# Optimization experiments

Hardware: AMD Instinct MI355X
Metric: run time of the kernel (lower is better)

The kernel has to match this reference:

```python
import jax, jax.numpy as jnp
import numpy as np

OBS, SEQ = 8, 12          # observed steps, predicted steps (seq_len init arg)
G, P = 96, 16             # scenes x pedestrians per scene (uniform groups)
B = G * P                 # 1536
H, E, BOT, MID = 128, 64, 1024, 512


def setup_inputs() -> dict:
    key = jax.random.key(0)
    ks = jax.random.split(key, 26)
    rn = lambda k, sh, s=0.05: jax.random.normal(k, sh, jnp.float32) * s
    starts = jnp.arange(G, dtype=jnp.int64) * P
    return {
        "obs_traj": rn(ks[0], (OBS, B, 2), 1.0),
        "obs_traj_rel": rn(ks[1], (OBS, B, 2), 1.0),
        "typeID_seq": rn(ks[2], (OBS, B, 1), 1.0),
        "h0": rn(ks[3], (1, B, H), 0.1),
        "c0": rn(ks[4], (1, B, H), 0.1),
        "seq_start_end": jnp.stack([starts, starts + P], axis=1),
        # decoder spatial embedding Linear(2, E)
        "W_emb": rn(ks[5], (E, 2)), "b_emb": rn(ks[6], (E,)),
        # LSTM(E, H) weights, gate order i,f,g,o (PyTorch convention)
        "W_ih": rn(ks[7], (4 * H, E)), "b_ih": rn(ks[8], (4 * H,)),
        "W_hh": rn(ks[9], (4 * H, H)), "b_hh": rn(ks[10], (4 * H,)),
        # hidden2pos Linear(H, 2)
        "W_pos": rn(ks[11], (2, H)), "b_pos": rn(ks[12], (2,)),
        # PoolHiddenNet: spatial_embedding Linear(2, E), mlp_pre_pool [E+H, 512, BOT]
        "Wp_emb": rn(ks[13], (E, 2)), "bp_emb": rn(ks[14], (E,)),
        "Wp1": rn(ks[15], (MID, E + H)), "bp1": rn(ks[16], (MID,)),
        "Wp2": rn(ks[17], (BOT, MID)), "bp2": rn(ks[18], (BOT,)),
        # Decoder mlp [H+BOT, mlp_dim, H]
        "Wm1": rn(ks[19], (1024, H + BOT)), "bm1": rn(ks[20], (1024,)),
        "Wm2": rn(ks[21], (H, 1024)), "bm2": rn(ks[22], (H,)),
    }


def _forward(obs_traj, obs_traj_rel, h0, c0,
             W_emb, b_emb, W_ih, b_ih, W_hh, b_hh, W_pos, b_pos,
             Wp_emb, bp_emb, Wp1, bp1, Wp2, bp2, Wm1, bm1, Wm2, bm2):
    batch = obs_traj.shape[1]

    def pool(h, pos):
        # uniform groups: h_states.view(-1,H)[start:end] == reshape to (G,P,H)
        hh = h.reshape(G, P, H)
        pp = pos.reshape(G, P, 2)
        # torch semantics: row (i,j) holds pos[j]-pos[i] and hidden[j]
        rel = pp[:, None, :, :] - pp[:, :, None, :]          # (G,Pi,Pj,2)
        emb = rel @ Wp_emb.T + bp_emb                        # (G,Pi,Pj,E)
        hb = jnp.broadcast_to(hh[:, None, :, :], (G, P, P, H))
        x = jnp.concatenate([emb, hb], axis=-1)              # (G,Pi,Pj,E+H)
        x = jax.nn.relu(x @ Wp1.T + bp1)
        x = jax.nn.relu(x @ Wp2.T + bp2)                     # (G,Pi,Pj,BOT)
        return x.max(axis=2).reshape(batch, BOT)             # max over neighbors j

    def step(carry, _):
        h, c, last_pos, dec_in = carry
        gates = dec_in @ W_ih.T + b_ih + h @ W_hh.T + b_hh
        i, f, g, o = jnp.split(gates, 4, axis=-1)
        c = jax.nn.sigmoid(f) * c + jax.nn.sigmoid(i) * jnp.tanh(g)
        h = jax.nn.sigmoid(o) * jnp.tanh(c)
        rel_pos = h @ W_pos.T + b_pos                        # (B,2)
        curr_pos = rel_pos + last_pos
        pool_h = pool(h, curr_pos)
        ctx = jnp.concatenate([h, pool_h], axis=-1)          # (B,H+BOT)
        h = jax.nn.relu(jax.nn.relu(ctx @ Wm1.T + bm1) @ Wm2.T + bm2)
        dec_in = rel_pos @ W_emb.T + b_emb
        return (h, c, curr_pos, dec_in), rel_pos

    dec_in0 = obs_traj_rel[-1] @ W_emb.T + b_emb
    carry0 = (h0[0], c0[0], obs_traj[-1], dec_in0)
    (h, c, _, _), rels = jax.lax.scan(step, carry0, None, length=SEQ)
    return rels, h[None]                                     # (SEQ,B,2), (1,B,H)


def reference(obs_traj, obs_traj_rel, typeID_seq, h0, c0, seq_start_end,
              W_emb, b_emb, W_ih, b_ih, W_hh, b_hh, W_pos, b_pos,
              Wp_emb, bp_emb, Wp1, bp1, Wp2, bp2, Wm1, bm1, Wm2, bm2):
    # typeID_seq / seq_start_end unused math-wise (typeID module off; groups uniform)
    return _forward(obs_traj, obs_traj_rel, h0, c0,
                    W_emb, b_emb, W_ih, b_ih, W_hh, b_hh, W_pos, b_pos,
                    Wp_emb, bp_emb, Wp1, bp1, Wp2, bp2, Wm1, bm1, Wm2, bm2)
```

## Files before the change

kernel.cpp:

```cpp
#include <hip/hip_runtime.h>
#include <math.h>

#define OBS 8
#define SEQL 12
#define G 96
#define PP 16
#define B 1536
#define HD 128
#define ED 64
#define BOT 1024
#define MIDD 512
#define CTXD (HD + BOT)
#define MLPH 1024

typedef __attribute__((ext_vector_type(8))) short bf16x8;
typedef __attribute__((ext_vector_type(4))) float f32x4;

__device__ inline short f2bf(float x) {
    union { float f; unsigned u; } v; v.f = x;
    unsigned r = v.u + 0x7fffu + ((v.u >> 16) & 1u);
    return (short)(r >> 16);
}

__global__ void swizzleB_kernel(const float* __restrict__ src, unsigned short* __restrict__ dst,
                                int NT, int K, int total) {
    int u = blockIdx.x * 256 + threadIdx.x;
    if (u >= total) return;
    int l = u & 63; int v = u >> 6; int nt = v % NT; int kt = v / NT;
    int n = nt * 16 + (l & 15);
    int k = kt * 32 + ((l >> 4) << 3);
    const float* s = src + n * K + k;
    float4 s0 = *(const float4*)s;
    float4 s1 = *(const float4*)(s + 4);
    bf16x8 o;
    o[0] = f2bf(s0.x); o[1] = f2bf(s0.y); o[2] = f2bf(s0.z); o[3] = f2bf(s0.w);
    o[4] = f2bf(s1.x); o[5] = f2bf(s1.y); o[6] = f2bf(s1.z); o[7] = f2bf(s1.w);
    *(bf16x8*)(dst + u * 8) = o;
}

__global__ void swizzle_cat_kernel(const float* __restrict__ W_ih, const float* __restrict__ W_hh,
                                   unsigned short* __restrict__ dst) {
    int u = blockIdx.x * 256 + threadIdx.x;
    if (u >= 6 * 32 * 64) return;
    int l = u & 63; int v = u >> 6; int nt = v & 31; int kt = v >> 5;
    int n = nt * 16 + (l & 15);
    int k0 = kt * 32 + ((l >> 4) << 3);
    bf16x8 o;
#pragma unroll
    for (int e = 0; e < 8; ++e) {
        int k = k0 + e;
        float val = (k < ED) ? W_ih[n * ED + k] : W_hh[n * HD + (k - ED)];
        o[e] = f2bf(val);
    }
    *(bf16x8*)(dst + u * 8) = o;
}

__global__ void swizzle_p1_kernel(const float* __restrict__ Wp1, const float* __restrict__ M0,
                                  const float* __restrict__ M1, const float* __restrict__ CV,
                                  unsigned short* __restrict__ dst) {
    int u = blockIdx.x * 256 + threadIdx.x;
    if (u >= 5 * 32 * 64) return;
    int l = u & 63; int v = u >> 6; int nt = v & 31; int kt = v >> 5;
    int n = nt * 16 + (l & 15);
    int k0 = kt * 32 + ((l >> 4) << 3);
    bf16x8 o;
#pragma unroll
    for (int e = 0; e < 8; ++e) {
        int k = k0 + e;
        float val;
        if (k < HD)       val = Wp1[n * (ED + HD) + ED + k];
        else if (k == HD)     val = M0[n];
        else if (k == HD + 1) val = M1[n];
        else if (k == HD + 2) val = CV[n];
        else                  val = 0.f;
        o[e] = f2bf(val);
    }
    *(bf16x8*)(dst + u * 8) = o;
}

__global__ void mcvec_kernel(const float* __restrict__ Wp1, const float* __restrict__ Wp_emb,
                             const float* __restrict__ bp_emb, const float* __restrict__ bp1,
                             float* __restrict__ M0, float* __restrict__ M1, float* __restrict__ CV) {
    int r = blockIdx.x * blockDim.x + threadIdx.x;
    if (r >= MIDD) return;
    float m0 = 0.f, m1 = 0.f, cv = 0.f;
    for (int e = 0; e < ED; ++e) {
        float w = Wp1[r * (ED + HD) + e];
        m0 += w * Wp_emb[e * 2 + 0];
        m1 += w * Wp_emb[e * 2 + 1];
        cv += w * bp_emb[e];
    }
    M0[r] = m0; M1[r] = m1; CV[r] = cv + bp1[r];
}

__global__ void init_kernel(const float* __restrict__ obs_traj, const float* __restrict__ obs_traj_rel,
                            const float* __restrict__ h0, const float* __restrict__ c0,
                            const float* __restrict__ W_emb, const float* __restrict__ b_emb,
                            float* __restrict__ Hb, float* __restrict__ Cb,
                            float* __restrict__ POSb, float* __restrict__ DIN) {
    int b = blockIdx.x;
    int t = threadIdx.x;
    Hb[b * HD + t] = h0[b * HD + t];
    Cb[b * HD + t] = c0[b * HD + t];
    if (t < 2) POSb[b * 2 + t] = obs_traj[((OBS - 1) * B + b) * 2 + t];
    if (t < ED) {
        float rx = obs_traj_rel[((OBS - 1) * B + b) * 2 + 0];
        float ry = obs_traj_rel[((OBS - 1) * B + b) * 2 + 1];
        DIN[b * ED + t] = W_emb[t * 2 + 0] * rx + W_emb[t * 2 + 1] * ry + b_emb[t];
    }
}

__global__ __launch_bounds__(512) void step_kernel(
    const unsigned short* __restrict__ WcatF, const float* __restrict__ b_ih,
    const float* __restrict__ b_hh,
    const float* __restrict__ W_pos, const float* __restrict__ b_pos,
    const float* __restrict__ W_emb, const float* __restrict__ b_emb,
    const unsigned short* __restrict__ Wp1F2,
    float* __restrict__ Hb, float* __restrict__ Cb, float* __restrict__ POSb,
    float* __restrict__ DIN, unsigned short* __restrict__ Hbf,
    float* __restrict__ Ab, float* __restrict__ rel_out) {

    __shared__ unsigned short gf[6 * 64 * 8];
    __shared__ unsigned short a2f[5 * 64 * 8];
    __shared__ float hsh[16 * HD];
    __shared__ float relsh[16][4];

    int gsc = blockIdx.x;
    int t = threadIdx.x;
    int lane = t & 63, w = t >> 6;
    int colid = lane & 15, quad = lane >> 4;

    if (t < 384) {
        int kt = t >> 6;
        int j = lane & 15;
        int b = gsc * PP + j;
        int k0 = kt * 32 + ((lane >> 4) << 3);
        float4 x0, x1;
        if (k0 < ED) {
            const float4* p = (const float4*)(DIN + b * ED + k0);
            x0 = p[0]; x1 = p[1];
        } else {
            const float4* p = (const float4*)(Hb + b * HD + (k0 - ED));
            x0 = p[0]; x1 = p[1];
        }
        bf16x8 o;
        o[0] = f2bf(x0.x); o[1] = f2bf(x0.y); o[2] = f2bf(x0.z); o[3] = f2bf(x0.w);
        o[4] = f2bf(x1.x); o[5] = f2bf(x1.y); o[6] = f2bf(x1.z); o[7] = f2bf(x1.w);
        *(bf16x8*)(gf + t * 8) = o;
    }
    __syncthreads();

    f32x4 acc[4];
#pragma unroll
    for (int gi = 0; gi < 4; ++gi) acc[gi] = (f32x4)0.f;
#pragma unroll
    for (int kt = 0; kt < 6; ++kt) {
        bf16x8 af = *(const bf16x8*)(gf + (kt * 64 + lane) * 8);
#pragma unroll
        for (int gi = 0; gi < 4; ++gi) {
            bf16x8 bfr = *(const bf16x8*)(WcatF + ((kt * 32 + gi * 8 + w) * 64 + lane) * 8);
            acc[gi] = __builtin_amdgcn_mfma_f32_16x16x32_bf16(af, bfr, acc[gi], 0, 0, 0);
        }
    }
    int hcol = w * 16 + colid;
    float bias[4];
#pragma unroll
    for (int gi = 0; gi < 4; ++gi) {
        int n = (gi * 8 + w) * 16 + colid;
        bias[gi] = b_ih[n] + b_hh[n];
    }
#pragma unroll
    for (int r = 0; r < 4; ++r) {
        int row = quad * 4 + r;
        int b = gsc * PP + row;
        float gI = acc[0][r] + bias[0];
        float gF = acc[1][r] + bias[1];
        float gG = acc[2][r] + bias[2];
        float gO = acc[3][r] + bias[3];
        float c = Cb[b * HD + hcol];
        float cn = (1.f / (1.f + expf(-gF))) * c + (1.f / (1.f + expf(-gI))) * tanhf(gG);
        float hn = (1.f / (1.f + expf(-gO))) * tanhf(cn);
        Cb[b * HD + hcol] = cn;
        Hbf[b * HD + hcol] = (unsigned short)f2bf(hn);
        hsh[row * HD + hcol] = hn;
    }
    __syncthreads();

    {
        int row = t >> 5, kk = t & 31;
        float r0 = 0.f, r1 = 0.f;
#pragma unroll
        for (int q = 0; q < 4; ++q) {
            int k = kk + q * 32;
            float hv = hsh[row * HD + k];
            r0 = fmaf(hv, W_pos[k], r0);
            r1 = fmaf(hv, W_pos[HD + k], r1);
        }
#pragma unroll
        for (int m = 16; m >= 1; m >>= 1) {
            r0 += __shfl_xor(r0, m, 64);
            r1 += __shfl_xor(r1, m, 64);
        }
        if (kk == 0) {
            int b = gsc * PP + row;
            r0 += b_pos[0]; r1 += b_pos[1];
            float px = POSb[b * 2 + 0] + r0;
            float py = POSb[b * 2 + 1] + r1;
            POSb[b * 2 + 0] = px; POSb[b * 2 + 1] = py;
            rel_out[b * 2 + 0] = r0; rel_out[b * 2 + 1] = r1;
            relsh[row][0] = r0; relsh[row][1] = r1; relsh[row][2] = px; relsh[row][3] = py;
        }
    }
    __syncthreads();

#pragma unroll
    for (int rep = 0; rep < 2; ++rep) {
        int idx = rep * 512 + t;
        int row = idx >> 6, e = idx & 63;
        int b = gsc * PP + row;
        DIN[b * ED + e] = W_emb[e * 2 + 0] * relsh[row][0] +
                          W_emb[e * 2 + 1] * relsh[row][1] + b_emb[e];
    }
    if (t < 320) {
        int kt = t >> 6;
        int j = lane & 15;
        int k0 = kt * 32 + ((lane >> 4) << 3);
        bf16x8 o;
#pragma unroll
        for (int e = 0; e < 8; ++e) {
            int k = k0 + e;
            float v;
            if (k < HD)            v = hsh[j * HD + k];
            else if (k == HD)      v = relsh[j][2];
            else if (k == HD + 1)  v = relsh[j][3];
            else if (k == HD + 2)  v = 1.f;
            else                   v = 0.f;
            o[e] = f2bf(v);
        }
        *(bf16x8*)(a2f + t * 8) = o;
    }
    __syncthreads();

    f32x4 acc2[4];
#pragma unroll
    for (int q = 0; q < 4; ++q) acc2[q] = (f32x4)0.f;
#pragma unroll
    for (int kt = 0; kt < 5; ++kt) {
        bf16x8 af = *(const bf16x8*)(a2f + (kt * 64 + lane) * 8);
#pragma unroll
        for (int q = 0; q < 4; ++q) {
            bf16x8 bfr = *(const bf16x8*)(Wp1F2 + ((kt * 32 + w * 4 + q) * 64 + lane) * 8);
            acc2[q] = __builtin_amdgcn_mfma_f32_16x16x32_bf16(af, bfr, acc2[q], 0, 0, 0);
        }
    }
#pragma unroll
    for (int q = 0; q < 4; ++q)
#pragma unroll
        for (int r = 0; r < 4; ++r) {
            int b = gsc * PP + quad * 4 + r;
            Ab[b * MIDD + (w * 4 + q) * 16 + colid] = acc2[q][r];
        }
}

__global__ __launch_bounds__(512) void pool_mfma2_kernel(
    const float* __restrict__ Ab, const float* __restrict__ POSb,
    const unsigned short* __restrict__ Wp2F, const float* __restrict__ bp2,
    const float* __restrict__ M0, const float* __restrict__ M1,
    unsigned short* __restrict__ POOLbf) {

    __shared__ float s_lds[4 * MIDD];
    __shared__ unsigned short af_lds[4 * 16 * 64 * 8];

    int bi = blockIdx.x;
    int g = bi >> 2, igrp = bi & 3;
    int t = threadIdx.x, lane = t & 63, w = t >> 6;

#pragma unroll
    for (int rep = 0; rep < 4; ++rep) {
        int idx = rep * 512 + t;
        int ii = idx >> 9, k = idx & 511;
        int i = g * PP + igrp * 4 + ii;
        s_lds[idx] = fmaf(M0[k], POSb[i * 2 + 0], M1[k] * POSb[i * 2 + 1]);
    }
    __syncthreads();
#pragma unroll
    for (int rep = 0; rep < 8; ++rep) {
        int u = rep * 512 + t;
        int ii = u >> 10, kt = (u >> 6) & 15, l = u & 63;
        int j = l & 15, k0 = kt * 32 + ((l >> 4) << 3);
        const float4* ap = (const float4*)(Ab + (g * PP + j) * MIDD + k0);
        float4 a0 = ap[0], a1 = ap[1];
        const float4* sp = (const float4*)(s_lds + ii * MIDD + k0);
        float4 s0 = sp[0], s1 = sp[1];
        bf16x8 o;
        o[0] = f2bf(fmaxf(a0.x - s0.x, 0.f));
        o[1] = f2bf(fmaxf(a0.y - s0.y, 0.f));
        o[2] = f2bf(fmaxf(a0.z - s0.z, 0.f));
        o[3] = f2bf(fmaxf(a0.w - s0.w, 0.f));
        o[4] = f2bf(fmaxf(a1.x - s1.x, 0.f));
        o[5] = f2bf(fmaxf(a1.y - s1.y, 0.f));
        o[6] = f2bf(fmaxf(a1.z - s1.z, 0.f));
        o[7] = f2bf(fmaxf(a1.w - s1.w, 0.f));
        *(bf16x8*)(af_lds + u * 8) = o;
    }
    __syncthreads();

    f32x4 acc[4][8];
#pragma unroll
    for (int ii = 0; ii < 4; ++ii)
#pragma unroll
        for (int n = 0; n < 8; ++n) acc[ii][n] = (f32x4)0.f;

    int ntb = w * 8;
    for (int kt = 0; kt < 16; ++kt) {
        bf16x8 bfr[8];
#pragma unroll
        for (int n = 0; n < 8; ++n)
            bfr[n] = *(const bf16x8*)(Wp2F + ((kt * 64 + ntb + n) * 64 + lane) * 8);
#pragma unroll
        for (int ii = 0; ii < 4; ++ii) {
            bf16x8 af = *(const bf16x8*)(af_lds + ((ii * 16 + kt) * 64 + lane) * 8);
#pragma unroll
            for (int n = 0; n < 8; ++n)
                acc[ii][n] = __builtin_amdgcn_mfma_f32_16x16x32_bf16(af, bfr[n], acc[ii][n], 0, 0, 0);
        }
    }

    int quad = lane >> 4, colid = lane & 15;
#pragma unroll
    for (int ii = 0; ii < 4; ++ii) {
        int i = igrp * 4 + ii;
#pragma unroll
        for (int n = 0; n < 8; ++n) {
            float m = fmaxf(fmaxf(acc[ii][n][0], acc[ii][n][1]),
                            fmaxf(acc[ii][n][2], acc[ii][n][3]));
            m = fmaxf(m, __shfl_xor(m, 16, 64));
            m = fmaxf(m, __shfl_xor(m, 32, 64));
            if (quad == 0) {
                int col = w * 128 + n * 16 + colid;
                float v = fmaxf(m + bp2[col], 0.f);
                POOLbf[(g * PP + i) * BOT + col] = (unsigned short)f2bf(v);
            }
        }
    }
}

__global__ __launch_bounds__(256) void mlp1_mfma_kernel(
    const unsigned short* __restrict__ Hbf, const unsigned short* __restrict__ POOLbf,
    const unsigned short* __restrict__ Wm1F, const float* __restrict__ bm1,
    unsigned short* __restrict__ Y1Mbf) {

    __shared__ unsigned short a_f[16 * 64 * 8];
    int mg = blockIdx.x;
    int ng = blockIdx.y;
    int t = threadIdx.x, lane = t & 63, w = t >> 6;
    int rh = w >> 1, nh = w & 1;

    f32x4 acc[2][2];
#pragma unroll
    for (int a = 0; a < 2; ++a)
#pragma unroll
        for (int b = 0; b < 2; ++b) acc[a][b] = (f32x4)0.f;

    for (int c = 0; c < 9; ++c) {
        __syncthreads();
#pragma unroll
        for (int u0 = 0; u0 < 1024; u0 += 256) {
            int u = u0 + t;
            int rg = u >> 8, kt = (u >> 6) & 3, l = u & 63;
            int row = mg * 64 + rg * 16 + (l & 15);
            int kl = kt * 32 + ((l >> 4) << 3);
            const unsigned short* src = (c == 0) ? (Hbf + row * HD + kl)
                                                 : (POOLbf + row * BOT + (c - 1) * 128 + kl);
            *(bf16x8*)(a_f + u * 8) = *(const bf16x8*)src;
        }
        __syncthreads();
#pragma unroll
        for (int kt = 0; kt < 4; ++kt) {
            int ktg = c * 4 + kt;
            bf16x8 bfr[2];
#pragma unroll
            for (int j = 0; j < 2; ++j) {
                int ntg = ng * 4 + nh * 2 + j;
                bfr[j] = *(const bf16x8*)(Wm1F + ((ktg * 64 + ntg) * 64 + lane) * 8);
            }
#pragma unroll
            for (int ri = 0; ri < 2; ++ri) {
                int rg = rh * 2 + ri;
                bf16x8 af = *(const bf16x8*)(a_f + ((rg * 4 + kt) * 64 + lane) * 8);
#pragma unroll
                for (int j = 0; j < 2; ++j)
                    acc[ri][j] = __builtin_amdgcn_mfma_f32_16x16x32_bf16(af, bfr[j], acc[ri][j], 0, 0, 0);
            }
        }
    }
    int quad = lane >> 4, colid = lane & 15;
#pragma unroll
    for (int ri = 0; ri < 2; ++ri)
#pragma unroll
        for (int j = 0; j < 2; ++j) {
            int col = ng * 64 + (nh * 2 + j) * 16 + colid;
            float bb = bm1[col];
#pragma unroll
            for (int r = 0; r < 4; ++r) {
                int row = mg * 64 + (rh * 2 + ri) * 16 + quad * 4 + r;
                float v = fmaxf(acc[ri][j][r] + bb, 0.f);
                Y1Mbf[row * MLPH + col] = (unsigned short)f2bf(v);
            }
        }
}

__global__ __launch_bounds__(256) void mlp2_mfma_kernel(
    const unsigned short* __restrict__ Y1Mbf, const unsigned short* __restrict__ Wm2F,
    const float* __restrict__ bm2, float* __restrict__ Hb, float* __restrict__ hout) {

    __shared__ unsigned short a_f[32 * 64 * 8];
    int rg = blockIdx.x;
    int t = threadIdx.x, lane = t & 63, w = t >> 6;

#pragma unroll
    for (int u0 = 0; u0 < 2048; u0 += 256) {
        int u = u0 + t;
        int kt = u >> 6, l = u & 63;
        int row = rg * 16 + (l & 15);
        int kl = kt * 32 + ((l >> 4) << 3);
        *(bf16x8*)(a_f + u * 8) = *(const bf16x8*)(Y1Mbf + row * MLPH + kl);
    }
    __syncthreads();

    f32x4 acc[2];
    acc[0] = (f32x4)0.f; acc[1] = (f32x4)0.f;
    for (int kt = 0; kt < 32; ++kt) {
        bf16x8 af = *(const bf16x8*)(a_f + (kt * 64 + lane) * 8);
#pragma unroll
        for (int j = 0; j < 2; ++j) {
            int ntg = w * 2 + j;
            bf16x8 bfr = *(const bf16x8*)(Wm2F + ((kt * 8 + ntg) * 64 + lane) * 8);
            acc[j] = __builtin_amdgcn_mfma_f32_16x16x32_bf16(af, bfr, acc[j], 0, 0, 0);
        }
    }
    int quad = lane >> 4, colid = lane & 15;
#pragma unroll
    for (int j = 0; j < 2; ++j) {
        int col = (w * 2 + j) * 16 + colid;
        float bb = bm2[col];
#pragma unroll
        for (int r = 0; r < 4; ++r) {
            int row = rg * 16 + quad * 4 + r;
            float v = fmaxf(acc[j][r] + bb, 0.f);
            Hb[row * HD + col] = v;
            if (hout) hout[row * HD + col] = v;
        }
    }
}

extern "C" void kernel_launch(void* const* d_in, const int* in_sizes, int n_in,
                              void* d_out, int out_size, void* d_ws, size_t ws_size,
                              hipStream_t stream) {
    const float* obs_traj     = (const float*)d_in[0];
    const float* obs_traj_rel = (const float*)d_in[1];
    const float* h0    = (const float*)d_in[3];
    const float* c0    = (const float*)d_in[4];
    const float* W_emb = (const float*)d_in[6];
    const float* b_emb = (const float*)d_in[7];
    const float* W_ih  = (const float*)d_in[8];
    const float* b_ih  = (const float*)d_in[9];
    const float* W_hh  = (const float*)d_in[10];
    const float* b_hh  = (const float*)d_in[11];
    const float* W_pos = (const float*)d_in[12];
    const float* b_pos = (const float*)d_in[13];
    const float* Wp_emb= (const float*)d_in[14];
    const float* bp_emb= (const float*)d_in[15];
    const float* Wp1   = (const float*)d_in[16];
    const float* bp1   = (const float*)d_in[17];
    const float* Wp2   = (const float*)d_in[18];
    const float* bp2   = (const float*)d_in[19];
    const float* Wm1   = (const float*)d_in[20];
    const float* bm1   = (const float*)d_in[21];
    const float* Wm2   = (const float*)d_in[22];
    const float* bm2   = (const float*)d_in[23];

    float* ws = (float*)d_ws;
    float* Hb    = ws; ws += B * HD;
    float* Cb    = ws; ws += B * HD;
    float* POSb  = ws; ws += B * 2;
    float* DIN   = ws; ws += B * ED;
    float* Ab    = ws; ws += B * MIDD;
    float* M0    = ws; ws += MIDD;
    float* M1    = ws; ws += MIDD;
    float* CV    = ws; ws += MIDD;
    unsigned short* us = (unsigned short*)ws;
    unsigned short* Hbf    = us; us += B * HD;
    unsigned short* POOLbf = us; us += B * BOT;
    unsigned short* Y1Mbf  = us; us += B * MLPH;
    unsigned short* WcatF  = us; us += 6 * 32 * 64 * 8;
    unsigned short* Wp1F2  = us; us += 5 * 32 * 64 * 8;
    unsigned short* Wp2F   = us; us += MIDD * BOT;
    unsigned short* Wm1F   = us; us += CTXD * MLPH;
    unsigned short* Wm2F   = us; us += MLPH * HD;

    float* out = (float*)d_out;
    float* rels_out = out;
    float* h_out    = out + SEQL * B * 2;

    {
        int tot = 16 * 64 * 64;
        swizzleB_kernel<<<(tot + 255) / 256, 256, 0, stream>>>(Wp2, Wp2F, 64, MIDD, tot);
        tot = 36 * 64 * 64;
        swizzleB_kernel<<<(tot + 255) / 256, 256, 0, stream>>>(Wm1, Wm1F, 64, CTXD, tot);
        tot = 32 * 8 * 64;
        swizzleB_kernel<<<(tot + 255) / 256, 256, 0, stream>>>(Wm2, Wm2F, 8, MLPH, tot);
        swizzle_cat_kernel<<<(6 * 32 * 64 + 255) / 256, 256, 0, stream>>>(W_ih, W_hh, WcatF);
    }
    mcvec_kernel<<<2, 256, 0, stream>>>(Wp1, Wp_emb, bp_emb, bp1, M0, M1, CV);
    swizzle_p1_kernel<<<(5 * 32 * 64 + 255) / 256, 256, 0, stream>>>(Wp1, M0, M1, CV, Wp1F2);
    init_kernel<<<B, 128, 0, stream>>>(obs_traj, obs_traj_rel, h0, c0, W_emb, b_emb,
                                       Hb, Cb, POSb, DIN);

    for (int s = 0; s < SEQL; ++s) {
        step_kernel<<<G, 512, 0, stream>>>(
            WcatF, b_ih, b_hh, W_pos, b_pos, W_emb, b_emb, Wp1F2,
            Hb, Cb, POSb, DIN, Hbf, Ab, rels_out + s * B * 2);
        pool_mfma2_kernel<<<G * 4, 512, 0, stream>>>(Ab, POSb, Wp2F, bp2, M0, M1, POOLbf);
        mlp1_mfma_kernel<<<dim3(24, 16), 256, 0, stream>>>(Hbf, POOLbf, Wm1F, bm1, Y1Mbf);
        mlp2_mfma_kernel<<<G, 256, 0, stream>>>(Y1Mbf, Wm2F, bm2, Hb,
                                                (s == SEQL - 1) ? h_out : (float*)nullptr);
    }
}
```

Baseline: 1.099 ms.

## Retile pool GEMM into more, smaller blocks with K-staged LDS passes

The pooling MFMA kernel now splits each scene into 16 blocks (2 row groups of 8 pedestrians by 8 column slices of 128) instead of 4 blocks covering all columns. The A operand is staged through LDS in four K passes, which cuts shared memory per block and drops the precomputed s_lds buffer in favour of recomputing M0*px+M1*py inline. The goal is more blocks and better occupancy (launch bounds 256,4) across the GPU's compute units. The cost is redundant A-tile construction, since each of the 8 column blocks rebuilds the same activations, plus more block barriers.

```diff
diff --git a/kernel.cpp b/kernel.cpp
--- a/kernel.cpp
+++ b/kernel.cpp
@@ -262,84 +262,95 @@
         }
 }
 
-__global__ __launch_bounds__(512) void pool_mfma2_kernel(
+__global__ __launch_bounds__(256, 4) void pool_mfma3_kernel(
     const float* __restrict__ Ab, const float* __restrict__ POSb,
     const unsigned short* __restrict__ Wp2F, const float* __restrict__ bp2,
     const float* __restrict__ M0, const float* __restrict__ M1,
     unsigned short* __restrict__ POOLbf) {
 
-    __shared__ float s_lds[4 * MIDD];
-    __shared__ unsigned short af_lds[4 * 16 * 64 * 8];
+    __shared__ unsigned short af_lds[8 * 4 * 64 * 8];
+    __shared__ float possh[8][2];
 
     int bi = blockIdx.x;
-    int g = bi >> 2, igrp = bi & 3;
+    int g = bi >> 4;
+    int sub = bi & 15;
+    int igrp = sub >> 3;
+    int colq = sub & 7;
     int t = threadIdx.x, lane = t & 63, w = t >> 6;
 
-#pragma unroll
-    for (int rep = 0; rep < 4; ++rep) {
-        int idx = rep * 512 + t;
-        int ii = idx >> 9, k = idx & 511;
-        int i = g * PP + igrp * 4 + ii;
-        s_lds[idx] = fmaf(M0[k], POSb[i * 2 + 0], M1[k] * POSb[i * 2 + 1]);
-    }
-    __syncthreads();
-#pragma unroll
-    for (int rep = 0; rep < 8; ++rep) {
-        int u = rep * 512 + t;
-        int ii = u >> 10, kt = (u >> 6) & 15, l = u & 63;
-        int j = l & 15, k0 = kt * 32 + ((l >> 4) << 3);
-        const float4* ap = (const float4*)(Ab + (g * PP + j) * MIDD + k0);
-        float4 a0 = ap[0], a1 = ap[1];
-        const float4* sp = (const float4*)(s_lds + ii * MIDD + k0);
-        float4 s0 = sp[0], s1 = sp[1];
-        bf16x8 o;
-        o[0] = f2bf(fmaxf(a0.x - s0.x, 0.f));
-        o[1] = f2bf(fmaxf(a0.y - s0.y, 0.f));
-        o[2] = f2bf(fmaxf(a0.z - s0.z, 0.f));
-        o[3] = f2bf(fmaxf(a0.w - s0.w, 0.f));
-        o[4] = f2bf(fmaxf(a1.x - s1.x, 0.f));
-        o[5] = f2bf(fmaxf(a1.y - s1.y, 0.f));
-        o[6] = f2bf(fmaxf(a1.z - s1.z, 0.f));
-        o[7] = f2bf(fmaxf(a1.w - s1.w, 0.f));
-        *(bf16x8*)(af_lds + u * 8) = o;
-    }
-    __syncthreads();
-
-    f32x4 acc[4][8];
-#pragma unroll
-    for (int ii = 0; ii < 4; ++ii)
-#pragma unroll
-        for (int n = 0; n < 8; ++n) acc[ii][n] = (f32x4)0.f;
-
-    int ntb = w * 8;
-    for (int kt = 0; kt < 16; ++kt) {
-        bf16x8 bfr[8];
-#pragma unroll
-        for (int n = 0; n < 8; ++n)
-            bfr[n] = *(const bf16x8*)(Wp2F + ((kt * 64 + ntb + n) * 64 + lane) * 8);
-#pragma unroll
-        for (int ii = 0; ii < 4; ++ii) {
-            bf16x8 af = *(const bf16x8*)(af_lds + ((ii * 16 + kt) * 64 + lane) * 8);
+    if (t < 16)
+        possh[t >> 1][t & 1] = POSb[(g * PP + igrp * 8 + (t >> 1)) * 2 + (t & 1)];
+
+    f32x4 acc[2][8];
+#pragma unroll
+    for (int p = 0; p < 2; ++p)
+#pragma unroll
+        for (int n = 0; n < 8; ++n) acc[p][n] = (f32x4)0.f;
+
+    const float* Ag = Ab + g * (PP * MIDD);
+    int ntb = colq * 8;
+
+    for (int pass = 0; pass < 4; ++pass) {
+        __syncthreads();
+#pragma unroll
+        for (int rep = 0; rep < 8; ++rep) {
+            int u = rep * 256 + t;
+            int ii = u >> 8;
+            int ktl = (u >> 6) & 3;
+            int l = u & 63;
+            int j = l & 15;
+            int k0 = (pass * 4 + ktl) * 32 + ((l >> 4) << 3);
+            const float4* ap = (const float4*)(Ag + j * MIDD + k0);
+            float4 a0 = ap[0], a1 = ap[1];
+            const float4* m0p = (const float4*)(M0 + k0);
+            const float4* m1p = (const float4*)(M1 + k0);
+            float4 m00 = m0p[0], m01 = m0p[1];
+            float4 m10 = m1p[0], m11 = m1p[1];
+            float px = possh[ii][0], py = possh[ii][1];
+            bf16x8 o;
+            o[0] = f2bf(fmaxf(a0.x - fmaf(m00.x, px, m10.x * py), 0.f));
+            o[1] = f2bf(fmaxf(a0.y - fmaf(m00.y, px, m10.y * py), 0.f));
+            o[2] = f2bf(fmaxf(a0.z - fmaf(m00.z, px, m10.z * py), 0.f));
+            o[3] = f2bf(fmaxf(a0.w - fmaf(m00.w, px, m10.w * py), 0.f));
+            o[4] = f2bf(fmaxf(a1.x - fmaf(m01.x, px, m11.x * py), 0.f));
+            o[5] = f2bf(fmaxf(a1.y - fmaf(m01.y, px, m11.y * py), 0.f));
+            o[6] = f2bf(fmaxf(a1.z - fmaf(m01.z, px, m11.z * py), 0.f));
+            o[7] = f2bf(fmaxf(a1.w - fmaf(m01.w, px, m11.w * py), 0.f));
+            *(bf16x8*)(af_lds + u * 8) = o;
+        }
+        __syncthreads();
+#pragma unroll
+        for (int ktl = 0; ktl < 4; ++ktl) {
+            int ktg = pass * 4 + ktl;
+            bf16x8 bfr[8];
 #pragma unroll
             for (int n = 0; n < 8; ++n)
-                acc[ii][n] = __builtin_amdgcn_mfma_f32_16x16x32_bf16(af, bfr[n], acc[ii][n], 0, 0, 0);
+                bfr[n] = *(const bf16x8*)(Wp2F + ((ktg * 64 + ntb + n) * 64 + lane) * 8);
+#pragma unroll
+            for (int p = 0; p < 2; ++p) {
+                int ii = w * 2 + p;
+                bf16x8 af = *(const bf16x8*)(af_lds + ((ii * 4 + ktl) * 64 + lane) * 8);
+#pragma unroll
+                for (int n = 0; n < 8; ++n)
+                    acc[p][n] = __builtin_amdgcn_mfma_f32_16x16x32_bf16(af, bfr[n], acc[p][n], 0, 0, 0);
+            }
         }
     }
 
     int quad = lane >> 4, colid = lane & 15;
 #pragma unroll
-    for (int ii = 0; ii < 4; ++ii) {
-        int i = igrp * 4 + ii;
+    for (int p = 0; p < 2; ++p) {
+        int i = g * PP + igrp * 8 + w * 2 + p;
 #pragma unroll
         for (int n = 0; n < 8; ++n) {
-            float m = fmaxf(fmaxf(acc[ii][n][0], acc[ii][n][1]),
-                            fmaxf(acc[ii][n][2], acc[ii][n][3]));
+            float m = fmaxf(fmaxf(acc[p][n][0], acc[p][n][1]),
+                            fmaxf(acc[p][n][2], acc[p][n][3]));
             m = fmaxf(m, __shfl_xor(m, 16, 64));
             m = fmaxf(m, __shfl_xor(m, 32, 64));
             if (quad == 0) {
-                int col = w * 128 + n * 16 + colid;
+                int col = colq * 128 + n * 16 + colid;
                 float v = fmaxf(m + bp2[col], 0.f);
-                POOLbf[(g * PP + i) * BOT + col] = (unsigned short)f2bf(v);
+                POOLbf[i * BOT + col] = (unsigned short)f2bf(v);
             }
         }
     }
@@ -521,7 +532,7 @@
         step_kernel<<<G, 512, 0, stream>>>(
             WcatF, b_ih, b_hh, W_pos, b_pos, W_emb, b_emb, Wp1F2,
             Hb, Cb, POSb, DIN, Hbf, Ab, rels_out + s * B * 2);
-        pool_mfma2_kernel<<<G * 4, 512, 0, stream>>>(Ab, POSb, Wp2F, bp2, M0, M1, POOLbf);
+        pool_mfma3_kernel<<<G * 16, 256, 0, stream>>>(Ab, POSb, Wp2F, bp2, M0, M1, POOLbf);
         mlp1_mfma_kernel<<<dim3(24, 16), 256, 0, stream>>>(Hbf, POOLbf, Wm1F, bm1, Y1Mbf);
         mlp2_mfma_kernel<<<G, 256, 0, stream>>>(Y1Mbf, Wm2F, bm2, Hb,
                                                 (s == SEQL - 1) ? h_out : (float*)nullptr);
```

Measured after the change: 1.326 ms. 1.21x slower.

## Split pooling into a bf16 operand-build kernel and a wider-grid pooling GEMM

Applied to the files above, without the earlier changes.

The fused pooling kernel, which built the relu(A - s) bf16 operands in LDS and ran the Wp2 GEMM with max-pool, becomes two kernels. The first writes the pre-swizzled operand tiles for every (group, i) to a global buffer (B*16*512 bf16, about 25 MB per step). The second runs the GEMM over 1536 smaller blocks, each covering 8 pedestrians and one eighth of the output columns, with launch_bounds(256,3) for occupancy. This gives more parallelism and less per-wave register pressure, but adds a large global write and read round trip plus an extra launch per step.

```diff
diff --git a/kernel.cpp b/kernel.cpp
--- a/kernel.cpp
+++ b/kernel.cpp
@@ -262,35 +262,35 @@
         }
 }
 
-__global__ __launch_bounds__(512) void pool_mfma2_kernel(
+__global__ __launch_bounds__(256) void build_y1_kernel(
     const float* __restrict__ Ab, const float* __restrict__ POSb,
-    const unsigned short* __restrict__ Wp2F, const float* __restrict__ bp2,
     const float* __restrict__ M0, const float* __restrict__ M1,
-    unsigned short* __restrict__ POOLbf) {
-
-    __shared__ float s_lds[4 * MIDD];
-    __shared__ unsigned short af_lds[4 * 16 * 64 * 8];
+    unsigned short* __restrict__ Y1F) {
+
+    __shared__ __align__(16) float s_lds[MIDD];
 
     int bi = blockIdx.x;
-    int g = bi >> 2, igrp = bi & 3;
-    int t = threadIdx.x, lane = t & 63, w = t >> 6;
-
+    int g = bi % 96;
+    int i = bi / 96;
+    int gi = g * PP + i;
+    int t = threadIdx.x;
+
+    float px = POSb[gi * 2 + 0], py = POSb[gi * 2 + 1];
+    s_lds[t]       = fmaf(M0[t], px, M1[t] * py);
+    s_lds[t + 256] = fmaf(M0[t + 256], px, M1[t + 256] * py);
+    __syncthreads();
+
+    const float* Ag = Ab + g * (PP * MIDD);
+    unsigned short* dst = Y1F + (size_t)gi * (16 * 64 * 8);
 #pragma unroll
     for (int rep = 0; rep < 4; ++rep) {
-        int idx = rep * 512 + t;
-        int ii = idx >> 9, k = idx & 511;
-        int i = g * PP + igrp * 4 + ii;
-        s_lds[idx] = fmaf(M0[k], POSb[i * 2 + 0], M1[k] * POSb[i * 2 + 1]);
-    }
-    __syncthreads();
-#pragma unroll
-    for (int rep = 0; rep < 8; ++rep) {
-        int u = rep * 512 + t;
-        int ii = u >> 10, kt = (u >> 6) & 15, l = u & 63;
-        int j = l & 15, k0 = kt * 32 + ((l >> 4) << 3);
-        const float4* ap = (const float4*)(Ab + (g * PP + j) * MIDD + k0);
+        int u = rep * 256 + t;
+        int kt = u >> 6, l = u & 63;
+        int j = l & 15;
+        int k0 = kt * 32 + ((l >> 4) << 3);
+        const float4* ap = (const float4*)(Ag + j * MIDD + k0);
         float4 a0 = ap[0], a1 = ap[1];
-        const float4* sp = (const float4*)(s_lds + ii * MIDD + k0);
+        const float4* sp = (const float4*)(s_lds + k0);
         float4 s0 = sp[0], s1 = sp[1];
         bf16x8 o;
         o[0] = f2bf(fmaxf(a0.x - s0.x, 0.f));
@@ -301,45 +301,67 @@
         o[5] = f2bf(fmaxf(a1.y - s1.y, 0.f));
         o[6] = f2bf(fmaxf(a1.z - s1.z, 0.f));
         o[7] = f2bf(fmaxf(a1.w - s1.w, 0.f));
-        *(bf16x8*)(af_lds + u * 8) = o;
-    }
-    __syncthreads();
-
-    f32x4 acc[4][8];
-#pragma unroll
-    for (int ii = 0; ii < 4; ++ii)
-#pragma unroll
-        for (int n = 0; n < 8; ++n) acc[ii][n] = (f32x4)0.f;
-
-    int ntb = w * 8;
+        *(bf16x8*)(dst + u * 8) = o;
+    }
+}
+
+__global__ __launch_bounds__(256, 3) void pool_gemm6_kernel(
+    const unsigned short* __restrict__ Y1F,
+    const unsigned short* __restrict__ Wp2F, const float* __restrict__ bp2,
+    unsigned short* __restrict__ POOLbf) {
+
+    int bi = blockIdx.x;
+    int g = bi % 96;
+    int rest = bi / 96;
+    int io = rest >> 3;
+    int colq = rest & 7;
+    int t = threadIdx.x, lane = t & 63, w = t >> 6;
+
+    int i0 = io * 8 + w * 2;
+    const unsigned short* a0p = Y1F + ((size_t)(g * PP + i0) * 16) * 512;
+    const unsigned short* a1p = a0p + 16 * 512;
+    int ntb = colq * 8;
+
+    f32x4 acc[2][8];
+#pragma unroll
+    for (int p = 0; p < 2; ++p)
+#pragma unroll
+        for (int n = 0; n < 8; ++n) acc[p][n] = (f32x4)0.f;
+
+#pragma unroll
     for (int kt = 0; kt < 16; ++kt) {
-        bf16x8 bfr[8];
-#pragma unroll
-        for (int n = 0; n < 8; ++n)
-            bfr[n] = *(const bf16x8*)(Wp2F + ((kt * 64 + ntb + n) * 64 + lane) * 8);
-#pragma unroll
-        for (int ii = 0; ii < 4; ++ii) {
-            bf16x8 af = *(const bf16x8*)(af_lds + ((ii * 16 + kt) * 64 + lane) * 8);
-#pragma unroll
-            for (int n = 0; n < 8; ++n)
-                acc[ii][n] = __builtin_amdgcn_mfma_f32_16x16x32_bf16(af, bfr[n], acc[ii][n], 0, 0, 0);
+        bf16x8 af0 = *(const bf16x8*)(a0p + (kt * 64 + lane) * 8);
+        bf16x8 af1 = *(const bf16x8*)(a1p + (kt * 64 + lane) * 8);
+#pragma unroll
+        for (int ng = 0; ng < 2; ++ng) {
+            bf16x8 bfr[4];
+#pragma unroll
+            for (int n = 0; n < 4; ++n)
+                bfr[n] = *(const bf16x8*)(Wp2F + ((kt * 64 + ntb + ng * 4 + n) * 64 + lane) * 8);
+#pragma unroll
+            for (int n = 0; n < 4; ++n) {
+                acc[0][ng * 4 + n] =
+                    __builtin_amdgcn_mfma_f32_16x16x32_bf16(af0, bfr[n], acc[0][ng * 4 + n], 0, 0, 0);
+                acc[1][ng * 4 + n] =
+                    __builtin_amdgcn_mfma_f32_16x16x32_bf16(af1, bfr[n], acc[1][ng * 4 + n], 0, 0, 0);
+            }
         }
     }
 
     int quad = lane >> 4, colid = lane & 15;
 #pragma unroll
-    for (int ii = 0; ii < 4; ++ii) {
-        int i = igrp * 4 + ii;
+    for (int p = 0; p < 2; ++p) {
+        int i = g * PP + i0 + p;
 #pragma unroll
         for (int n = 0; n < 8; ++n) {
-            float m = fmaxf(fmaxf(acc[ii][n][0], acc[ii][n][1]),
-                            fmaxf(acc[ii][n][2], acc[ii][n][3]));
+            float m = fmaxf(fmaxf(acc[p][n][0], acc[p][n][1]),
+                            fmaxf(acc[p][n][2], acc[p][n][3]));
             m = fmaxf(m, __shfl_xor(m, 16, 64));
             m = fmaxf(m, __shfl_xor(m, 32, 64));
             if (quad == 0) {
-                int col = w * 128 + n * 16 + colid;
+                int col = (ntb + n) * 16 + colid;
                 float v = fmaxf(m + bp2[col], 0.f);
-                POOLbf[(g * PP + i) * BOT + col] = (unsigned short)f2bf(v);
+                POOLbf[i * BOT + col] = (unsigned short)f2bf(v);
             }
         }
     }
@@ -498,6 +520,7 @@
     unsigned short* Wp2F   = us; us += MIDD * BOT;
     unsigned short* Wm1F   = us; us += CTXD * MLPH;
     unsigned short* Wm2F   = us; us += MLPH * HD;
+    unsigned short* Y1F    = us; us += (size_t)B * 16 * 64 * 8;
 
     float* out = (float*)d_out;
     float* rels_out = out;
@@ -521,7 +544,8 @@
         step_kernel<<<G, 512, 0, stream>>>(
             WcatF, b_ih, b_hh, W_pos, b_pos, W_emb, b_emb, Wp1F2,
             Hb, Cb, POSb, DIN, Hbf, Ab, rels_out + s * B * 2);
-        pool_mfma2_kernel<<<G * 4, 512, 0, stream>>>(Ab, POSb, Wp2F, bp2, M0, M1, POOLbf);
+        build_y1_kernel<<<B, 256, 0, stream>>>(Ab, POSb, M0, M1, Y1F);
+        pool_gemm6_kernel<<<G * 16, 256, 0, stream>>>(Y1F, Wp2F, bp2, POOLbf);
         mlp1_mfma_kernel<<<dim3(24, 16), 256, 0, stream>>>(Hbf, POOLbf, Wm1F, bm1, Y1Mbf);
         mlp2_mfma_kernel<<<G, 256, 0, stream>>>(Y1Mbf, Wm2F, bm2, Hb,
                                                 (s == SEQL - 1) ? h_out : (float*)nullptr);
```

Result: slower. 1.185 ms (+7.9%).
